# Kernel tuning notes

Hardware: AMD Instinct MI355X
Metric: run time of the kernel (lower is better)

## Reference

```python
import jax, jax.numpy as jnp
import numpy as np

D_MODEL = 1024
NUM_HEADS = 16
D_K = D_MODEL // NUM_HEADS
B, L = 2, 4096


def setup_inputs() -> dict:
    key = jax.random.key(0)
    ks = jax.random.split(key, 12)
    s = 0.02
    return {
        "q": jax.random.normal(ks[0], (B, L, D_MODEL), dtype=jnp.float32),
        "k": jax.random.normal(ks[1], (B, L, D_MODEL), dtype=jnp.float32),
        "v": jax.random.normal(ks[2], (B, L, D_MODEL), dtype=jnp.float32),
        "Wq": jax.random.normal(ks[3], (D_MODEL, D_MODEL), dtype=jnp.float32) * s,
        "bq": jax.random.normal(ks[4], (D_MODEL,), dtype=jnp.float32) * s,
        "Wk": jax.random.normal(ks[5], (D_MODEL, D_MODEL), dtype=jnp.float32) * s,
        "bk": jax.random.normal(ks[6], (D_MODEL,), dtype=jnp.float32) * s,
        "Wv": jax.random.normal(ks[7], (D_MODEL, D_MODEL), dtype=jnp.float32) * s,
        "bv": jax.random.normal(ks[8], (D_MODEL,), dtype=jnp.float32) * s,
        "Wo": jax.random.normal(ks[9], (D_MODEL, D_MODEL), dtype=jnp.float32) * s,
        "bo": jax.random.normal(ks[10], (D_MODEL,), dtype=jnp.float32) * s,
    }


def reference(q, k, v, Wq, bq, Wk, bk, Wv, bv, Wo, bo):
    b, l, _ = q.shape
    # projections (torch Linear: x @ W.T + b), reshape to [b, l, h, d]
    qf = (q @ Wq.T + bq).reshape(b, l, NUM_HEADS, D_K)
    kf = (k @ Wk.T + bk).reshape(b, l, NUM_HEADS, D_K)
    vf = (v @ Wv.T + bv).reshape(b, l, NUM_HEADS, D_K)
    # elu+1 feature map (positive features)
    qf = jax.nn.elu(qf) + 1.0
    kf = jax.nn.elu(kf) + 1.0
    # normalizer uses full-sequence k sum (as in the original code)
    z = 1.0 / (jnp.einsum("blhd,bhd->blh", qf, kf.sum(axis=1)) + 1e-6)
    # cumulative sums over sequence (the linear-attention scan state)
    k_cum = jnp.cumsum(kf, axis=1)  # [b, l, h, d]
    v_cum = jnp.cumsum(vf, axis=1)  # [b, l, h, d]
    context = jnp.einsum("blhd,blhd->blh", qf, k_cum)  # [b, l, h]
    context = context[..., None] * v_cum * z[..., None]  # [b, l, h, d]
    context = context.reshape(b, l, NUM_HEADS * D_K)
    return context @ Wo.T + bo
```

## Files before the change

kernel.cpp:

```cpp
#include <hip/hip_runtime.h>
#include <hip/hip_bf16.h>
#include <cstdint>
#include <cstddef>

#define D_MODEL 1024
#define NUM_HEADS 16
#define DK_DIM 64
#define BATCH 2
#define SEQ 4096
#define MROWS (BATCH*SEQ)
#define NCHUNK 128
#define CHUNK 32

#define BM 256
#define BN 128
#define BK 64
#define NSLOT 3
#define SLOT_SH (BM*BK + BN*BK)
#define KTILES (D_MODEL/BK)

typedef __attribute__((ext_vector_type(4))) float f32x4;
typedef __attribute__((ext_vector_type(2))) float f32x2;
typedef __attribute__((ext_vector_type(8))) short bf16x8;
typedef __attribute__((ext_vector_type(4))) short s16x4;
typedef __attribute__((ext_vector_type(2))) uint32_t u32x2;
typedef __attribute__((ext_vector_type(4))) uint32_t u32x4;

__device__ __forceinline__ float b2f(short s) {
  union { uint32_t u; float f; } c; c.u = ((uint32_t)(uint16_t)s) << 16; return c.f;
}
__device__ __forceinline__ short f2b(float f) {
  union { float f; uint32_t u; } c; c.f = f;
  uint32_t u = c.u;
  u += 0x7FFFu + ((u >> 16) & 1u);
  return (short)(u >> 16);
}
__device__ __forceinline__ f32x4 b4_to_f4(s16x4 s) {
  f32x4 r;
  r.x = b2f(s.x); r.y = b2f(s.y); r.z = b2f(s.z); r.w = b2f(s.w);
  return r;
}
__device__ __forceinline__ uint32_t cvtpk(float lo, float hi) {
  uint32_t r;
  asm("v_cvt_pk_bf16_f32 %0, %1, %2" : "=v"(r) : "v"(lo), "v"(hi));
  return r;
}

__global__ __launch_bounds__(256) void cvt_w4(
    const float* __restrict__ s0, const float* __restrict__ s1,
    const float* __restrict__ s2, const float* __restrict__ s3,
    short* __restrict__ dst) {
  const int y = blockIdx.y;
  const float* s = (y == 0) ? s0 : (y == 1) ? s1 : (y == 2) ? s2 : s3;
  const int i = blockIdx.x * 256 + threadIdx.x;
  float4 v = reinterpret_cast<const float4*>(s)[i];
  s16x4 o;
  o.x = f2b(v.x); o.y = f2b(v.y); o.z = f2b(v.z); o.w = f2b(v.w);
  reinterpret_cast<s16x4*>(dst)[(size_t)y * (D_MODEL * D_MODEL / 4) + i] = o;
}

template<int AFP32, int OUTBF16>
__global__ __launch_bounds__(512, 2) void gemm8(
    const void* __restrict__ A0, const void* __restrict__ A1,
    const void* __restrict__ A2, const short* __restrict__ Wbase,
    const float* __restrict__ b0, const float* __restrict__ b1,
    const float* __restrict__ b2, void* __restrict__ Cbase, int actmask)
{
  extern __shared__ __align__(16) short lds[];
  const int tid = threadIdx.x;
  const int wid = tid >> 6;
  const int lane = tid & 63;
  const int brow = blockIdx.x * BM;
  const int bcol = blockIdx.y * BN;
  const int z = blockIdx.z;
  const int wr = wid >> 1, wc = wid & 1;

  const void* Ap = (z == 0) ? A0 : (z == 1) ? A1 : A2;
  const float* bias = (z == 0) ? b0 : (z == 1) ? b1 : b2;
  const short* Bw = Wbase + (size_t)z * D_MODEL * D_MODEL;
  const int act = (actmask >> z) & 1;
  const float* __restrict__ A32 = (const float*)Ap;
  const short* __restrict__ A16 = (const short*)Ap;

  f32x4 acc[4][4];
#pragma unroll
  for (int i = 0; i < 4; ++i)
#pragma unroll
    for (int j = 0; j < 4; ++j)
#pragma unroll
      for (int t = 0; t < 4; ++t) acc[i][j][t] = 0.f;

  const int srow = lane >> 3;
  const int gql  = lane & 7;
  const int sgel = (gql ^ srow) * 8;

  auto stageB = [&](int t) {
    short* sB = lds + (t % NSLOT) * SLOT_SH + BM * BK;
    const int k0 = t * BK;
#pragma unroll
    for (int i = 0; i < 2; ++i) {
      const int r = i * 64 + wid * 8;
      const short* g = Bw + (size_t)(bcol + r + srow) * D_MODEL + k0 + sgel;
      __builtin_amdgcn_global_load_lds((const __attribute__((address_space(1))) void*)g,
          (__attribute__((address_space(3))) void*)(sB + r * BK), 16, 0, 0);
    }
  };
  auto stageA16 = [&](int t) {
    short* sA = lds + (t % NSLOT) * SLOT_SH;
    const int k0 = t * BK;
#pragma unroll
    for (int i = 0; i < 4; ++i) {
      const int r = i * 64 + wid * 8;
      const short* g = A16 + (size_t)(brow + r + srow) * D_MODEL + k0 + sgel;
      __builtin_amdgcn_global_load_lds((const __attribute__((address_space(1))) void*)g,
          (__attribute__((address_space(3))) void*)(sA + r * BK), 16, 0, 0);
    }
  };
  auto loadA32 = [&](int t, float4 (&buf)[8]) {
    const int k0 = t * BK;
#pragma unroll
    for (int i = 0; i < 4; ++i) {
      const float* src = A32 + (size_t)(brow + i * 64 + wid * 8 + srow) * D_MODEL + k0 + gql * 8;
      buf[2 * i]     = *reinterpret_cast<const float4*>(src);
      buf[2 * i + 1] = *reinterpret_cast<const float4*>(src + 4);
    }
  };
  auto writeA32 = [&](int t, float4 (&buf)[8]) {
    char* sA = (char*)(lds + (t % NSLOT) * SLOT_SH);
#pragma unroll
    for (int i = 0; i < 4; ++i) {
      u32x4 w;
      w.x = cvtpk(buf[2 * i].x,     buf[2 * i].y);
      w.y = cvtpk(buf[2 * i].z,     buf[2 * i].w);
      w.z = cvtpk(buf[2 * i + 1].x, buf[2 * i + 1].y);
      w.w = cvtpk(buf[2 * i + 1].z, buf[2 * i + 1].w);
      const int ebyte = (i * 64 + wid * 8 + srow) * 128 + ((gql ^ srow) * 16);
      *reinterpret_cast<u32x4*>(sA + ebyte) = w;
    }
  };

  const int lane15 = lane & 15;
  const int swz = (lane & 7) << 4;
  const int kq = (lane >> 4) * 16;

  auto compute = [&](int t) {
    const char* sAb = (const char*)(lds + (t % NSLOT) * SLOT_SH);
    const char* sBb = sAb + BM * BK * 2;
    auto rdA = [&](int mi, int ks) -> bf16x8 {
      const int row = wr * 64 + mi * 16 + lane15;
      const int off = row * 128 + ((ks * 64 + kq) ^ swz);
      return *reinterpret_cast<const bf16x8*>(sAb + off);
    };
    auto rdB = [&](int nj, int ks) -> bf16x8 {
      const int row = wc * 64 + nj * 16 + lane15;
      const int off = row * 128 + ((ks * 64 + kq) ^ swz);
      return *reinterpret_cast<const bf16x8*>(sBb + off);
    };
    bf16x8 Af[2][2], Bf[2][2][2];
#pragma unroll
    for (int m2 = 0; m2 < 2; ++m2)
#pragma unroll
      for (int ks = 0; ks < 2; ++ks) Af[m2][ks] = rdA(m2, ks);
#pragma unroll
    for (int j2 = 0; j2 < 2; ++j2)
#pragma unroll
      for (int ks = 0; ks < 2; ++ks) Bf[0][j2][ks] = rdB(j2, ks);
#pragma unroll
    for (int m2 = 0; m2 < 2; ++m2)
#pragma unroll
      for (int j2 = 0; j2 < 2; ++j2)
#pragma unroll
        for (int ks = 0; ks < 2; ++ks)
          acc[m2][j2] = __builtin_amdgcn_mfma_f32_16x16x32_bf16(Bf[0][j2][ks], Af[m2][ks], acc[m2][j2], 0, 0, 0);
#pragma unroll
    for (int j2 = 0; j2 < 2; ++j2)
#pragma unroll
      for (int ks = 0; ks < 2; ++ks) Bf[1][j2][ks] = rdB(2 + j2, ks);
#pragma unroll
    for (int m2 = 0; m2 < 2; ++m2)
#pragma unroll
      for (int j2 = 0; j2 < 2; ++j2)
#pragma unroll
        for (int ks = 0; ks < 2; ++ks)
          acc[m2][2 + j2] = __builtin_amdgcn_mfma_f32_16x16x32_bf16(Bf[1][j2][ks], Af[m2][ks], acc[m2][2 + j2], 0, 0, 0);
#pragma unroll
    for (int m2 = 0; m2 < 2; ++m2)
#pragma unroll
      for (int ks = 0; ks < 2; ++ks) Af[m2][ks] = rdA(2 + m2, ks);
#pragma unroll
    for (int m2 = 0; m2 < 2; ++m2)
#pragma unroll
      for (int j2 = 0; j2 < 2; ++j2)
#pragma unroll
        for (int ks = 0; ks < 2; ++ks)
          acc[2 + m2][2 + j2] = __builtin_amdgcn_mfma_f32_16x16x32_bf16(Bf[1][j2][ks], Af[m2][ks], acc[2 + m2][2 + j2], 0, 0, 0);
#pragma unroll
    for (int m2 = 0; m2 < 2; ++m2)
#pragma unroll
      for (int j2 = 0; j2 < 2; ++j2)
#pragma unroll
        for (int ks = 0; ks < 2; ++ks)
          acc[2 + m2][j2] = __builtin_amdgcn_mfma_f32_16x16x32_bf16(Bf[0][j2][ks], Af[m2][ks], acc[2 + m2][j2], 0, 0, 0);
  };

  if constexpr (AFP32) {
    float4 buf0[8], buf1[8];
    loadA32(0, buf0);
    asm volatile("s_waitcnt vmcnt(0)" ::: "memory");
    writeA32(0, buf0);
    loadA32(1, buf1);
    stageB(0); stageB(1);

    auto body = [&](int t, float4 (&bufW)[8], float4 (&bufL)[8]) {
      if (t == KTILES - 1) { asm volatile("s_waitcnt vmcnt(0)" ::: "memory"); }
      else                 { asm volatile("s_waitcnt vmcnt(2)" ::: "memory"); }
      if (t + 1 < KTILES) writeA32(t + 1, bufW);
      if (t + 2 < KTILES) loadA32(t + 2, bufL);
      asm volatile("s_waitcnt lgkmcnt(0)" ::: "memory");
      __builtin_amdgcn_s_barrier();
      __builtin_amdgcn_sched_barrier(0);
      if (t + 2 < KTILES) stageB(t + 2);
      compute(t);
    };
#pragma unroll 1
    for (int t2 = 0; t2 < KTILES; t2 += 2) {
      body(t2,     buf1, buf0);
      body(t2 + 1, buf0, buf1);
    }
  } else {
    stageA16(0); stageB(0);
    stageA16(1); stageB(1);
#pragma unroll 1
    for (int t = 0; t < KTILES; ++t) {
      if (t == KTILES - 1) { asm volatile("s_waitcnt vmcnt(0)" ::: "memory"); }
      else                 { asm volatile("s_waitcnt vmcnt(6)" ::: "memory"); }
      __builtin_amdgcn_s_barrier();
      __builtin_amdgcn_sched_barrier(0);
      if (t + 2 < KTILES) { stageA16(t + 2); stageB(t + 2); }
      compute(t);
    }
  }

  const int csub4 = (lane >> 4) * 4;
#pragma unroll
  for (int mi = 0; mi < 4; ++mi) {
    const int row = brow + wr * 64 + mi * 16 + lane15;
    const size_t rowbase = (size_t)z * MROWS * D_MODEL + (size_t)row * D_MODEL;
#pragma unroll
    for (int nj = 0; nj < 4; ++nj) {
      const int col0 = bcol + wc * 64 + nj * 16 + csub4;
      const float4 bv = *reinterpret_cast<const float4*>(&bias[col0]);
      float v0 = acc[mi][nj][0] + bv.x;
      float v1 = acc[mi][nj][1] + bv.y;
      float v2 = acc[mi][nj][2] + bv.z;
      float v3 = acc[mi][nj][3] + bv.w;
      if (act) {
        v0 = (v0 > 0.f) ? (v0 + 1.f) : __expf(v0);
        v1 = (v1 > 0.f) ? (v1 + 1.f) : __expf(v1);
        v2 = (v2 > 0.f) ? (v2 + 1.f) : __expf(v2);
        v3 = (v3 > 0.f) ? (v3 + 1.f) : __expf(v3);
      }
      if (OUTBF16) {
        u32x2 w;
        w.x = cvtpk(v0, v1);
        w.y = cvtpk(v2, v3);
        *reinterpret_cast<u32x2*>(&((short*)Cbase)[rowbase + col0]) = w;
      } else {
        float4 w; w.x = v0; w.y = v1; w.z = v2; w.w = v3;
        *reinterpret_cast<float4*>(&((float*)Cbase)[rowbase + col0]) = w;
      }
    }
  }
}

__global__ __launch_bounds__(256) void chunk_sums(
    const short* __restrict__ kf, const short* __restrict__ vf,
    float* __restrict__ ck, float* __restrict__ cv)
{
  const int gw = blockIdx.x * 4 + (threadIdx.x >> 6);
  const int lane = threadIdx.x & 63;
  const int c = gw & (NCHUNK - 1);
  const int h = (gw >> 7) & (NUM_HEADS - 1);
  const int b = gw >> 11;
  const int half = lane >> 5;
  const int dpair = (lane & 31) * 2;
  const size_t base = ((size_t)(b * SEQ + c * CHUNK) * NUM_HEADS + h) * DK_DIM + dpair;

  float skx = 0.f, sky = 0.f, svx = 0.f, svy = 0.f;
#pragma unroll
  for (int i = 0; i < CHUNK / 2; ++i) {
    const size_t off = base + (size_t)(2 * i + half) * D_MODEL;
    uint32_t ku = *reinterpret_cast<const uint32_t*>(&kf[off]);
    uint32_t vu = *reinterpret_cast<const uint32_t*>(&vf[off]);
    skx += b2f((short)(ku & 0xffff)); sky += b2f((short)(ku >> 16));
    svx += b2f((short)(vu & 0xffff)); svy += b2f((short)(vu >> 16));
  }
  skx += __shfl_xor(skx, 32, 64); sky += __shfl_xor(sky, 32, 64);
  svx += __shfl_xor(svx, 32, 64); svy += __shfl_xor(svy, 32, 64);
  if (half == 0) {
    const size_t o = ((size_t)((b * NUM_HEADS + h) * NCHUNK + c)) * DK_DIM + dpair;
    f32x2 a; a.x = skx; a.y = sky;
    f32x2 bb; bb.x = svx; bb.y = svy;
    *reinterpret_cast<f32x2*>(&ck[o]) = a;
    *reinterpret_cast<f32x2*>(&cv[o]) = bb;
  }
}

__global__ __launch_bounds__(64) void chunk_scan(
    float* __restrict__ ck, float* __restrict__ cv, float* __restrict__ ksum)
{
  const int bh = blockIdx.x;
  const int d = threadIdx.x;
  float rk = 0.f, rv = 0.f;
#pragma unroll 8
  for (int c = 0; c < NCHUNK; ++c) {
    const size_t o = ((size_t)(bh * NCHUNK + c)) * DK_DIM + d;
    const float tk = ck[o], tv = cv[o];
    ck[o] = rk; cv[o] = rv;
    rk += tk; rv += tv;
  }
  ksum[bh * DK_DIM + d] = rk;
}

__global__ __launch_bounds__(256) void scan_ctx(
    const short* __restrict__ qf, const short* __restrict__ kf,
    const short* __restrict__ vf,
    const float* __restrict__ ck, const float* __restrict__ cv,
    const float* __restrict__ ksum, short* __restrict__ ctx)
{
  const int gw = blockIdx.x * 4 + (threadIdx.x >> 6);
  const int lane = threadIdx.x & 63;
  const int pg = lane >> 4;
  const int dg = lane & 15;
  const int c = gw & (NCHUNK - 1);
  const int h = (gw >> 7) & (NUM_HEADS - 1);
  const int b = gw >> 11;
  const int bh = b * NUM_HEADS + h;
  const int d4 = dg * 4;

  f32x4 krun = *reinterpret_cast<const f32x4*>(
      &ck[((size_t)(bh * NCHUNK + c)) * DK_DIM + d4]);
  f32x4 vrun = *reinterpret_cast<const f32x4*>(
      &cv[((size_t)(bh * NCHUNK + c)) * DK_DIM + d4]);
  const f32x4 kst = *reinterpret_cast<const f32x4*>(&ksum[bh * DK_DIM + d4]);

  const size_t base = ((size_t)(b * SEQ + c * CHUNK) * NUM_HEADS + h) * DK_DIM + d4;

  for (int p0 = 0; p0 < CHUNK; p0 += 4) {
    const size_t qoff = base + (size_t)(p0 + pg) * D_MODEL;
    const f32x4 q4 = b4_to_f4(*reinterpret_cast<const s16x4*>(&qf[qoff]));
    f32x4 sk, sv;
#pragma unroll
    for (int i = 0; i < 4; ++i) {
      const size_t off = base + (size_t)(p0 + i) * D_MODEL;
      krun += b4_to_f4(*reinterpret_cast<const s16x4*>(&kf[off]));
      vrun += b4_to_f4(*reinterpret_cast<const s16x4*>(&vf[off]));
      if (i == pg) { sk = krun; sv = vrun; }
    }
    float s1 = q4.x * sk.x + q4.y * sk.y + q4.z * sk.z + q4.w * sk.w;
    float s2 = q4.x * kst.x + q4.y * kst.y + q4.z * kst.z + q4.w * kst.w;
#pragma unroll
    for (int m = 1; m < 16; m <<= 1) {
      s1 += __shfl_xor(s1, m, 64);
      s2 += __shfl_xor(s2, m, 64);
    }
    const float g = s1 / (s2 + 1e-6f);
    s16x4 o;
    o.x = f2b(g * sv.x); o.y = f2b(g * sv.y);
    o.z = f2b(g * sv.z); o.w = f2b(g * sv.w);
    *reinterpret_cast<s16x4*>(&ctx[qoff]) = o;
  }
}

extern "C" void kernel_launch(void* const* d_in, const int* in_sizes, int n_in,
                              void* d_out, int out_size, void* d_ws, size_t ws_size,
                              hipStream_t stream) {
  const float* q  = (const float*)d_in[0];
  const float* k  = (const float*)d_in[1];
  const float* v  = (const float*)d_in[2];
  const float* Wq = (const float*)d_in[3];
  const float* bq = (const float*)d_in[4];
  const float* Wk = (const float*)d_in[5];
  const float* bk = (const float*)d_in[6];
  const float* Wv = (const float*)d_in[7];
  const float* bv = (const float*)d_in[8];
  const float* Wo = (const float*)d_in[9];
  const float* bo = (const float*)d_in[10];
  float* out = (float*)d_out;

  uint8_t* p = (uint8_t*)d_ws;
  auto alloc = [&](size_t bytes) { uint8_t* r = p; p += bytes; return r; };
  short* qf  = (short*)alloc((size_t)MROWS * D_MODEL * 2);
  short* kf  = (short*)alloc((size_t)MROWS * D_MODEL * 2);
  short* vf  = (short*)alloc((size_t)MROWS * D_MODEL * 2);
  short* ctx = (short*)alloc((size_t)MROWS * D_MODEL * 2);
  short* Wqb = (short*)alloc((size_t)D_MODEL * D_MODEL * 2);
  short* Wkb = (short*)alloc((size_t)D_MODEL * D_MODEL * 2);
  short* Wvb = (short*)alloc((size_t)D_MODEL * D_MODEL * 2);
  short* Wob = (short*)alloc((size_t)D_MODEL * D_MODEL * 2);
  float* ck   = (float*)alloc((size_t)BATCH * NUM_HEADS * NCHUNK * DK_DIM * 4);
  float* cv   = (float*)alloc((size_t)BATCH * NUM_HEADS * NCHUNK * DK_DIM * 4);
  float* ksum = (float*)alloc((size_t)BATCH * NUM_HEADS * DK_DIM * 4);
  (void)Wkb; (void)Wvb;

  const dim3 gproj(MROWS / BM, D_MODEL / BN, 3);
  const dim3 gout (MROWS / BM, D_MODEL / BN, 1);
  const int shbytes = NSLOT * SLOT_SH * (int)sizeof(short);

  (void)hipFuncSetAttribute((const void*)gemm8<1, 1>,
      hipFuncAttributeMaxDynamicSharedMemorySize, shbytes);
  (void)hipFuncSetAttribute((const void*)gemm8<0, 0>,
      hipFuncAttributeMaxDynamicSharedMemorySize, shbytes);

  cvt_w4<<<dim3(D_MODEL * D_MODEL / 4 / 256, 4), 256, 0, stream>>>(Wq, Wk, Wv, Wo, Wqb);

  gemm8<1, 1><<<gproj, 512, shbytes, stream>>>(q, k, v, Wqb, bq, bk, bv, qf, 0x3);

  chunk_sums<<<BATCH * NUM_HEADS * NCHUNK / 4, 256, 0, stream>>>(kf, vf, ck, cv);
  chunk_scan<<<BATCH * NUM_HEADS, 64, 0, stream>>>(ck, cv, ksum);
  scan_ctx<<<BATCH * NUM_HEADS * NCHUNK / 4, 256, 0, stream>>>(qf, kf, vf, ck, cv, ksum, ctx);

  gemm8<0, 0><<<gout, 512, shbytes, stream>>>(ctx, ctx, ctx, Wob, bo, bo, bo, out, 0);
}
```

Measured before the change: 140.8 us.

## Replace 3-stage swizzled 256x128 GEMM with single-buffered 128x128 tile kernel

Rewrites the projection and output GEMMs to use 128x128 tiles with 256 threads and a single static LDS buffer, dropping the 3-slot async pipeline and XOR swizzle. A tiles are loaded via registers for both fp32 and bf16 inputs, B tiles through direct-to-LDS loads, with two barriers per k-tile. The aim is more blocks in flight and simpler code. The costs are lost overlap of memory and compute, and possible LDS bank conflicts without swizzling.

```diff
diff --git a/kernel.cpp b/kernel.cpp
--- a/kernel.cpp
+++ b/kernel.cpp
@@ -12,11 +12,9 @@
 #define NCHUNK 128
 #define CHUNK 32
 
-#define BM 256
+#define BM 128
 #define BN 128
 #define BK 64
-#define NSLOT 3
-#define SLOT_SH (BM*BK + BN*BK)
 #define KTILES (D_MODEL/BK)
 
 typedef __attribute__((ext_vector_type(4))) float f32x4;
@@ -60,13 +58,13 @@
 }
 
 template<int AFP32, int OUTBF16>
-__global__ __launch_bounds__(512, 2) void gemm8(
+__global__ __launch_bounds__(256, 3) void gemm4(
     const void* __restrict__ A0, const void* __restrict__ A1,
     const void* __restrict__ A2, const short* __restrict__ Wbase,
     const float* __restrict__ b0, const float* __restrict__ b1,
     const float* __restrict__ b2, void* __restrict__ Cbase, int actmask)
 {
-  extern __shared__ __align__(16) short lds[];
+  __shared__ short lds[(BM + BN) * BK];
   const int tid = threadIdx.x;
   const int wid = tid >> 6;
   const int lane = tid & 63;
@@ -92,153 +90,96 @@
 
   const int srow = lane >> 3;
   const int gql  = lane & 7;
-  const int sgel = (gql ^ srow) * 8;
-
+
+  float4 abuf32[8];
+  u32x4  abuf16[4];
+
+  auto loadA = [&](int t) {
+    const int k0 = t * BK;
+#pragma unroll
+    for (int i = 0; i < 4; ++i) {
+      const int row = brow + i * 32 + wid * 8 + srow;
+      if constexpr (AFP32) {
+        const float* src = A32 + (size_t)row * D_MODEL + k0 + gql * 8;
+        abuf32[2 * i]     = *reinterpret_cast<const float4*>(src);
+        abuf32[2 * i + 1] = *reinterpret_cast<const float4*>(src + 4);
+      } else {
+        abuf16[i] = *reinterpret_cast<const u32x4*>(A16 + (size_t)row * D_MODEL + k0 + gql * 8);
+      }
+    }
+  };
+  auto writeA = [&]() {
+#pragma unroll
+    for (int i = 0; i < 4; ++i) {
+      u32x4 w;
+      if constexpr (AFP32) {
+        w.x = cvtpk(abuf32[2 * i].x,     abuf32[2 * i].y);
+        w.y = cvtpk(abuf32[2 * i].z,     abuf32[2 * i].w);
+        w.z = cvtpk(abuf32[2 * i + 1].x, abuf32[2 * i + 1].y);
+        w.w = cvtpk(abuf32[2 * i + 1].z, abuf32[2 * i + 1].w);
+      } else {
+        w = abuf16[i];
+      }
+      const int ebyte = (i * 32 + wid * 8 + srow) * 128 + gql * 16;
+      *reinterpret_cast<u32x4*>((char*)lds + ebyte) = w;
+    }
+  };
   auto stageB = [&](int t) {
-    short* sB = lds + (t % NSLOT) * SLOT_SH + BM * BK;
+    short* sB = lds + BM * BK;
     const int k0 = t * BK;
 #pragma unroll
-    for (int i = 0; i < 2; ++i) {
-      const int r = i * 64 + wid * 8;
-      const short* g = Bw + (size_t)(bcol + r + srow) * D_MODEL + k0 + sgel;
+    for (int i = 0; i < 4; ++i) {
+      const int r = i * 32 + wid * 8;
+      const short* g = Bw + (size_t)(bcol + r + srow) * D_MODEL + k0 + gql * 8;
       __builtin_amdgcn_global_load_lds((const __attribute__((address_space(1))) void*)g,
           (__attribute__((address_space(3))) void*)(sB + r * BK), 16, 0, 0);
     }
   };
-  auto stageA16 = [&](int t) {
-    short* sA = lds + (t % NSLOT) * SLOT_SH;
-    const int k0 = t * BK;
-#pragma unroll
-    for (int i = 0; i < 4; ++i) {
-      const int r = i * 64 + wid * 8;
-      const short* g = A16 + (size_t)(brow + r + srow) * D_MODEL + k0 + sgel;
-      __builtin_amdgcn_global_load_lds((const __attribute__((address_space(1))) void*)g,
-          (__attribute__((address_space(3))) void*)(sA + r * BK), 16, 0, 0);
+
+  const int lane15 = lane & 15;
+  const int kq = (lane >> 4) * 16;
+
+  auto compute = [&]() {
+    const char* sAb = (const char*)lds;
+    const char* sBb = sAb + BM * BK * 2;
+#pragma unroll
+    for (int ks = 0; ks < 2; ++ks) {
+      bf16x8 Af[4], Bf[4];
+#pragma unroll
+      for (int mi = 0; mi < 4; ++mi)
+        Af[mi] = *reinterpret_cast<const bf16x8*>(
+            sAb + (wr * 64 + mi * 16 + lane15) * 128 + ks * 64 + kq);
+#pragma unroll
+      for (int nj = 0; nj < 4; ++nj)
+        Bf[nj] = *reinterpret_cast<const bf16x8*>(
+            sBb + (wc * 64 + nj * 16 + lane15) * 128 + ks * 64 + kq);
+#pragma unroll
+      for (int mi = 0; mi < 4; ++mi)
+#pragma unroll
+        for (int nj = 0; nj < 4; ++nj)
+          acc[mi][nj] = __builtin_amdgcn_mfma_f32_16x16x32_bf16(Bf[nj], Af[mi], acc[mi][nj], 0, 0, 0);
     }
   };
-  auto loadA32 = [&](int t, float4 (&buf)[8]) {
-    const int k0 = t * BK;
-#pragma unroll
-    for (int i = 0; i < 4; ++i) {
-      const float* src = A32 + (size_t)(brow + i * 64 + wid * 8 + srow) * D_MODEL + k0 + gql * 8;
-      buf[2 * i]     = *reinterpret_cast<const float4*>(src);
-      buf[2 * i + 1] = *reinterpret_cast<const float4*>(src + 4);
-    }
-  };
-  auto writeA32 = [&](int t, float4 (&buf)[8]) {
-    char* sA = (char*)(lds + (t % NSLOT) * SLOT_SH);
-#pragma unroll
-    for (int i = 0; i < 4; ++i) {
-      u32x4 w;
-      w.x = cvtpk(buf[2 * i].x,     buf[2 * i].y);
-      w.y = cvtpk(buf[2 * i].z,     buf[2 * i].w);
-      w.z = cvtpk(buf[2 * i + 1].x, buf[2 * i + 1].y);
-      w.w = cvtpk(buf[2 * i + 1].z, buf[2 * i + 1].w);
-      const int ebyte = (i * 64 + wid * 8 + srow) * 128 + ((gql ^ srow) * 16);
-      *reinterpret_cast<u32x4*>(sA + ebyte) = w;
-    }
-  };
-
-  const int lane15 = lane & 15;
-  const int swz = (lane & 7) << 4;
-  const int kq = (lane >> 4) * 16;
-
-  auto compute = [&](int t) {
-    const char* sAb = (const char*)(lds + (t % NSLOT) * SLOT_SH);
-    const char* sBb = sAb + BM * BK * 2;
-    auto rdA = [&](int mi, int ks) -> bf16x8 {
-      const int row = wr * 64 + mi * 16 + lane15;
-      const int off = row * 128 + ((ks * 64 + kq) ^ swz);
-      return *reinterpret_cast<const bf16x8*>(sAb + off);
-    };
-    auto rdB = [&](int nj, int ks) -> bf16x8 {
-      const int row = wc * 64 + nj * 16 + lane15;
-      const int off = row * 128 + ((ks * 64 + kq) ^ swz);
-      return *reinterpret_cast<const bf16x8*>(sBb + off);
-    };
-    bf16x8 Af[2][2], Bf[2][2][2];
-#pragma unroll
-    for (int m2 = 0; m2 < 2; ++m2)
-#pragma unroll
-      for (int ks = 0; ks < 2; ++ks) Af[m2][ks] = rdA(m2, ks);
-#pragma unroll
-    for (int j2 = 0; j2 < 2; ++j2)
-#pragma unroll
-      for (int ks = 0; ks < 2; ++ks) Bf[0][j2][ks] = rdB(j2, ks);
-#pragma unroll
-    for (int m2 = 0; m2 < 2; ++m2)
-#pragma unroll
-      for (int j2 = 0; j2 < 2; ++j2)
-#pragma unroll
-        for (int ks = 0; ks < 2; ++ks)
-          acc[m2][j2] = __builtin_amdgcn_mfma_f32_16x16x32_bf16(Bf[0][j2][ks], Af[m2][ks], acc[m2][j2], 0, 0, 0);
-#pragma unroll
-    for (int j2 = 0; j2 < 2; ++j2)
-#pragma unroll
-      for (int ks = 0; ks < 2; ++ks) Bf[1][j2][ks] = rdB(2 + j2, ks);
-#pragma unroll
-    for (int m2 = 0; m2 < 2; ++m2)
-#pragma unroll
-      for (int j2 = 0; j2 < 2; ++j2)
-#pragma unroll
-        for (int ks = 0; ks < 2; ++ks)
-          acc[m2][2 + j2] = __builtin_amdgcn_mfma_f32_16x16x32_bf16(Bf[1][j2][ks], Af[m2][ks], acc[m2][2 + j2], 0, 0, 0);
-#pragma unroll
-    for (int m2 = 0; m2 < 2; ++m2)
-#pragma unroll
-      for (int ks = 0; ks < 2; ++ks) Af[m2][ks] = rdA(2 + m2, ks);
-#pragma unroll
-    for (int m2 = 0; m2 < 2; ++m2)
-#pragma unroll
-      for (int j2 = 0; j2 < 2; ++j2)
-#pragma unroll
-        for (int ks = 0; ks < 2; ++ks)
-          acc[2 + m2][2 + j2] = __builtin_amdgcn_mfma_f32_16x16x32_bf16(Bf[1][j2][ks], Af[m2][ks], acc[2 + m2][2 + j2], 0, 0, 0);
-#pragma unroll
-    for (int m2 = 0; m2 < 2; ++m2)
-#pragma unroll
-      for (int j2 = 0; j2 < 2; ++j2)
-#pragma unroll
-        for (int ks = 0; ks < 2; ++ks)
-          acc[2 + m2][j2] = __builtin_amdgcn_mfma_f32_16x16x32_bf16(Bf[0][j2][ks], Af[m2][ks], acc[2 + m2][j2], 0, 0, 0);
-  };
-
-  if constexpr (AFP32) {
-    float4 buf0[8], buf1[8];
-    loadA32(0, buf0);
-    asm volatile("s_waitcnt vmcnt(0)" ::: "memory");
-    writeA32(0, buf0);
-    loadA32(1, buf1);
-    stageB(0); stageB(1);
-
-    auto body = [&](int t, float4 (&bufW)[8], float4 (&bufL)[8]) {
-      if (t == KTILES - 1) { asm volatile("s_waitcnt vmcnt(0)" ::: "memory"); }
-      else                 { asm volatile("s_waitcnt vmcnt(2)" ::: "memory"); }
-      if (t + 1 < KTILES) writeA32(t + 1, bufW);
-      if (t + 2 < KTILES) loadA32(t + 2, bufL);
-      asm volatile("s_waitcnt lgkmcnt(0)" ::: "memory");
-      __builtin_amdgcn_s_barrier();
-      __builtin_amdgcn_sched_barrier(0);
-      if (t + 2 < KTILES) stageB(t + 2);
-      compute(t);
-    };
+
+  loadA(0);
 #pragma unroll 1
-    for (int t2 = 0; t2 < KTILES; t2 += 2) {
-      body(t2,     buf1, buf0);
-      body(t2 + 1, buf0, buf1);
-    }
-  } else {
-    stageA16(0); stageB(0);
-    stageA16(1); stageB(1);
-#pragma unroll 1
-    for (int t = 0; t < KTILES; ++t) {
-      if (t == KTILES - 1) { asm volatile("s_waitcnt vmcnt(0)" ::: "memory"); }
-      else                 { asm volatile("s_waitcnt vmcnt(6)" ::: "memory"); }
-      __builtin_amdgcn_s_barrier();
-      __builtin_amdgcn_sched_barrier(0);
-      if (t + 2 < KTILES) { stageA16(t + 2); stageB(t + 2); }
-      compute(t);
-    }
+  for (int t = 0; t < KTILES; ++t) {
+    asm volatile("s_waitcnt lgkmcnt(0)" ::: "memory");
+    __builtin_amdgcn_s_barrier();
+    stageB(t);
+    asm volatile("s_waitcnt vmcnt(4)" ::: "memory");
+    writeA();
+    if (t + 1 < KTILES) loadA(t + 1);
+    asm volatile("s_waitcnt lgkmcnt(0)" ::: "memory");
+    if (t + 1 < KTILES) {
+      if constexpr (AFP32) asm volatile("s_waitcnt vmcnt(8)" ::: "memory");
+      else                 asm volatile("s_waitcnt vmcnt(4)" ::: "memory");
+    } else {
+      asm volatile("s_waitcnt vmcnt(0)" ::: "memory");
+    }
+    __builtin_amdgcn_s_barrier();
+    __builtin_amdgcn_sched_barrier(0);
+    compute();
   }
 
   const int csub4 = (lane >> 4) * 4;
@@ -405,20 +346,14 @@
 
   const dim3 gproj(MROWS / BM, D_MODEL / BN, 3);
   const dim3 gout (MROWS / BM, D_MODEL / BN, 1);
-  const int shbytes = NSLOT * SLOT_SH * (int)sizeof(short);
-
-  (void)hipFuncSetAttribute((const void*)gemm8<1, 1>,
-      hipFuncAttributeMaxDynamicSharedMemorySize, shbytes);
-  (void)hipFuncSetAttribute((const void*)gemm8<0, 0>,
-      hipFuncAttributeMaxDynamicSharedMemorySize, shbytes);
 
   cvt_w4<<<dim3(D_MODEL * D_MODEL / 4 / 256, 4), 256, 0, stream>>>(Wq, Wk, Wv, Wo, Wqb);
 
-  gemm8<1, 1><<<gproj, 512, shbytes, stream>>>(q, k, v, Wqb, bq, bk, bv, qf, 0x3);
+  gemm4<1, 1><<<gproj, 256, 0, stream>>>(q, k, v, Wqb, bq, bk, bv, qf, 0x3);
 
   chunk_sums<<<BATCH * NUM_HEADS * NCHUNK / 4, 256, 0, stream>>>(kf, vf, ck, cv);
   chunk_scan<<<BATCH * NUM_HEADS, 64, 0, stream>>>(ck, cv, ksum);
   scan_ctx<<<BATCH * NUM_HEADS * NCHUNK / 4, 256, 0, stream>>>(qf, kf, vf, ck, cv, ksum, ctx);
 
-  gemm8<0, 0><<<gout, 512, shbytes, stream>>>(ctx, ctx, ctx, Wob, bo, bo, bo, out, 0);
-}
+  gemm4<0, 0><<<gout, 256, 0, stream>>>(ctx, ctx, ctx, Wob, bo, bo, bo, out, 0);
+}
```

Measured after the change: 150.5 us. 1.07x slower.
